# Kernel optimization log

Measured on AMD Instinct MI355X. Metric: run time of the kernel, lower is better.

## Reference

```python
import jax, jax.numpy as jnp
import numpy as np

INPUT_SIZE = 128
HID = 64
B, T = 256, 1024

def setup_inputs() -> dict:
    key = jax.random.key(0)
    ks = jax.random.split(key, 12)
    s1 = 1.0 / np.sqrt(HID)
    def u(k, shape):
        return jax.random.uniform(k, shape, jnp.float32, -s1, s1)
    return {
        "x": jax.random.normal(ks[0], (B, T, INPUT_SIZE), jnp.float32),
        "w_ih0": u(ks[1], (4 * HID, INPUT_SIZE)),
        "w_hh0": u(ks[2], (4 * HID, HID)),
        "b_ih0": u(ks[3], (4 * HID,)),
        "b_hh0": u(ks[4], (4 * HID,)),
        "w_ih1": u(ks[5], (4 * HID, HID)),
        "w_hh1": u(ks[6], (4 * HID, HID)),
        "b_ih1": u(ks[7], (4 * HID,)),
        "b_hh1": u(ks[8], (4 * HID,)),
        "w_out": u(ks[9], (1, HID)),
        "b_out": u(ks[10], (1,)),
    }

def _lstm(x, w_ih, w_hh, b_ih, b_hh):
    # x: [B, T, I] -> h sequence [B, T, H]; PyTorch gate order i, f, g, o
    Bb = x.shape[0]
    H = w_hh.shape[1]
    # precompute input contribution for all timesteps (one big GEMM)
    xg = jnp.einsum('bti,gi->btg', x, w_ih) + b_ih + b_hh  # [B, T, 4H]
    def step(carry, g_t):
        h, c = carry
        g = g_t + h @ w_hh.T  # [B, 4H]
        i, f, gg, o = jnp.split(g, 4, axis=-1)
        i = jax.nn.sigmoid(i)
        f = jax.nn.sigmoid(f)
        gg = jnp.tanh(gg)
        o = jax.nn.sigmoid(o)
        c = f * c + i * gg
        h = o * jnp.tanh(c)
        return (h, c), h
    init = (jnp.zeros((Bb, H), x.dtype), jnp.zeros((Bb, H), x.dtype))
    _, hs = jax.lax.scan(step, init, jnp.swapaxes(xg, 0, 1))  # [T, B, H]
    return jnp.swapaxes(hs, 0, 1)

def reference(x, w_ih0, w_hh0, b_ih0, b_hh0, w_ih1, w_hh1, b_ih1, b_hh1, w_out, b_out):
    h1 = _lstm(x, w_ih0, w_hh0, b_ih0, b_hh0)   # [B, T, H]
    h2 = _lstm(h1, w_ih1, w_hh1, b_ih1, b_hh1)  # [B, T, H]
    logits = jnp.einsum('bth,oh->bto', h2, w_out) + b_out  # [B, T, 1]
    return jax.nn.sigmoid(logits)
```

## Files before the change

kernel.cpp:

```cpp
#include <hip/hip_runtime.h>

#define BB 256
#define TT 1024
#define II 128
#define HH 64
#define BT (BB * TT)

typedef _Float16 h2 __attribute__((ext_vector_type(2)));
typedef _Float16 half8 __attribute__((ext_vector_type(8)));
typedef float f32x4 __attribute__((ext_vector_type(4)));
typedef unsigned int uint;
typedef unsigned short ushort;

#define BC(u) __builtin_bit_cast(h2, (uint)(u))
#define MFMA16(a, b, c) __builtin_amdgcn_mfma_f32_16x16x32_f16((a), (b), (c), 0, 0, 0)
#define SIG(v) __builtin_amdgcn_rcpf(1.0f + __expf(-(v)))
#define TNH(v) (1.0f - 2.0f * __builtin_amdgcn_rcpf(1.0f + __expf(2.0f * (v))))

#define BAR() asm volatile("s_waitcnt lgkmcnt(0)\n\ts_barrier" ::: "memory")

__device__ __forceinline__ uint pk2(float a, float b) {
    h2 h; h[0] = (_Float16)a; h[1] = (_Float16)b;
    return __builtin_bit_cast(uint, h);
}

__global__ __launch_bounds__(256) __attribute__((amdgpu_waves_per_eu(1, 1)))
void lstm2_core(const float* __restrict__ x, const float* __restrict__ w_ih0,
                const float* __restrict__ w_hh0,
                const float* __restrict__ b_ih0, const float* __restrict__ b_hh0,
                const float* __restrict__ w_ih1, const float* __restrict__ w_hh1,
                const float* __restrict__ b_ih1, const float* __restrict__ b_hh1,
                ushort* __restrict__ h1g)
{
    const int bb = blockIdx.x;
    const int w  = threadIdx.x >> 6;
    const int j  = threadIdx.x & 63;
    const int qq = j >> 4, cc = j & 15;
    const int j4 = j * 4;

    __shared__ __align__(16) uint   h0buf[8][32];
    __shared__ __align__(16) uint   h1buf[32];
    __shared__ __align__(16) float  zbuf[8][64][4];
    __shared__ __align__(16) ushort xgb[2][16][264];
    __shared__ __align__(16) uint4  wfrag[16][4][4][16];

    {
        #pragma unroll
        for (int t = 0; t < 16; ++t) {
            const int flat = t * 16 + cc;
            const int srcrow = (flat & 3) * 64 + (flat >> 2);
            const float* p = w_ih0 + (size_t)srcrow * II + w * 32 + qq * 8;
            uint4 v;
            v.x = pk2(p[0], p[1]); v.y = pk2(p[2], p[3]);
            v.z = pk2(p[4], p[5]); v.w = pk2(p[6], p[7]);
            wfrag[t][w][qq][cc] = v;
        }
    }
    __syncthreads();

    uint4 Bf[16][2];
    if (w < 3) {
        const float* Wsel = (w == 0) ? w_hh0 : (w == 1) ? w_ih1 : w_hh1;
        #pragma unroll
        for (int t = 0; t < 16; ++t) {
            const int row = (t & 3) * 64 + (t >> 2) * 16 + cc;
            const float* rp = Wsel + (size_t)row * 64 + qq * 8;
            #pragma unroll
            for (int kh = 0; kh < 2; ++kh) {
                const float* p = rp + kh * 32;
                uint4 v;
                v.x = pk2(p[0], p[1]); v.y = pk2(p[2], p[3]);
                v.z = pk2(p[4], p[5]); v.w = pk2(p[6], p[7]);
                Bf[t][kh] = v;
            }
        }
    }

    float bI = 0.f, bF = 0.f, bG = 0.f, bO = 0.f;
    if (w == 0) {
        bI = b_ih0[j]       + b_hh0[j];
        bF = b_ih0[64 + j]  + b_hh0[64 + j];
        bG = b_ih0[128 + j] + b_hh0[128 + j];
        bO = b_ih0[192 + j] + b_hh0[192 + j];
    } else if (w == 2) {
        bI = b_ih1[j]       + b_hh1[j];
        bF = b_ih1[64 + j]  + b_hh1[64 + j];
        bG = b_ih1[128 + j] + b_hh1[128 + j];
        bO = b_ih1[192 + j] + b_hh1[192 + j];
    }

    float cst = 0.0f;
    const float* xrow = x + (size_t)bb * TT * II;
    ushort* h1b = h1g + (size_t)bb * TT * 64 + j;

    const f32x4 ZR4 = {0.f, 0.f, 0.f, 0.f};
    const int qlo = qq & 1, qhi = qq >> 1;

    half8 af0 = {0,0,0,0,0,0,0,0}, af1 = {0,0,0,0,0,0,0,0};
    f32x4 zr = {0.f, 0.f, 0.f, 0.f};

    float4 xr[8];
    half8 wa0 = {0,0,0,0,0,0,0,0}, wa1 = wa0, wa2 = wa0, wa3 = wa0;

#define XLOAD(WND) if ((WND) < 64) { \
    const float* xp_ = xrow + (size_t)((WND) * 16 + cc) * II + qq * 8; \
    xr[0] = *(const float4*)(xp_ +  0); xr[1] = *(const float4*)(xp_ +  4); \
    xr[2] = *(const float4*)(xp_ + 32); xr[3] = *(const float4*)(xp_ + 36); \
    xr[4] = *(const float4*)(xp_ + 64); xr[5] = *(const float4*)(xp_ + 68); \
    xr[6] = *(const float4*)(xp_ + 96); xr[7] = *(const float4*)(xp_ + 100); }

#define MKAF4() { uint4 u_; \
    u_.x = pk2(xr[0].x, xr[0].y); u_.y = pk2(xr[0].z, xr[0].w); \
    u_.z = pk2(xr[1].x, xr[1].y); u_.w = pk2(xr[1].z, xr[1].w); \
    wa0 = __builtin_bit_cast(half8, u_); \
    u_.x = pk2(xr[2].x, xr[2].y); u_.y = pk2(xr[2].z, xr[2].w); \
    u_.z = pk2(xr[3].x, xr[3].y); u_.w = pk2(xr[3].z, xr[3].w); \
    wa1 = __builtin_bit_cast(half8, u_); \
    u_.x = pk2(xr[4].x, xr[4].y); u_.y = pk2(xr[4].z, xr[4].w); \
    u_.z = pk2(xr[5].x, xr[5].y); u_.w = pk2(xr[5].z, xr[5].w); \
    wa2 = __builtin_bit_cast(half8, u_); \
    u_.x = pk2(xr[6].x, xr[6].y); u_.y = pk2(xr[6].z, xr[6].w); \
    u_.z = pk2(xr[7].x, xr[7].y); u_.w = pk2(xr[7].z, xr[7].w); \
    wa3 = __builtin_bit_cast(half8, u_); }

#define WTILE(TILE, BUF) { \
    f32x4 d_ = ZR4; \
    d_ = MFMA16(wa0, __builtin_bit_cast(half8, wfrag[TILE][0][qq][cc]), d_); \
    d_ = MFMA16(wa1, __builtin_bit_cast(half8, wfrag[TILE][1][qq][cc]), d_); \
    d_ = MFMA16(wa2, __builtin_bit_cast(half8, wfrag[TILE][2][qq][cc]), d_); \
    d_ = MFMA16(wa3, __builtin_bit_cast(half8, wfrag[TILE][3][qq][cc]), d_); \
    _Pragma("unroll") \
    for (int r_ = 0; r_ < 4; ++r_) { \
        _Float16 hv_ = (_Float16)d_[r_]; \
        xgb[BUF][qq * 4 + r_][(TILE) * 16 + cc] = __builtin_bit_cast(ushort, hv_); } }

    if (w == 3) {
        XLOAD(0)
        MKAF4()
        #pragma unroll
        for (int t = 0; t < 16; ++t) WTILE(t, 0)
        XLOAD(1)
    }
    __syncthreads();

#define LDAF(SRC) { const char* hb_ = (const char*)(SRC); \
    af0 = *(const half8*)(hb_ + (qq << 4)); \
    af1 = *(const half8*)(hb_ + 64 + (qq << 4)); }

#define GEMV16(SI, SF, SG, SO) { \
    f32x4 D[16]; \
    _Pragma("unroll") \
    for (int t = 0; t < 16; ++t) { \
        f32x4 d_ = MFMA16(af0, __builtin_bit_cast(half8, Bf[t][0]), ZR4); \
        D[t] = MFMA16(af1, __builtin_bit_cast(half8, Bf[t][1]), d_); } \
    { float a_, b_; \
      a_ = qlo ? D[ 4][0] : D[ 0][0]; b_ = qlo ? D[12][0] : D[ 8][0]; SI = qhi ? b_ : a_; \
      a_ = qlo ? D[ 5][0] : D[ 1][0]; b_ = qlo ? D[13][0] : D[ 9][0]; SF = qhi ? b_ : a_; \
      a_ = qlo ? D[ 6][0] : D[ 2][0]; b_ = qlo ? D[14][0] : D[10][0]; SG = qhi ? b_ : a_; \
      a_ = qlo ? D[ 7][0] : D[ 3][0]; b_ = qlo ? D[15][0] : D[11][0]; SO = qhi ? b_ : a_; } }

#define PSTEP(KK) \
    if ((KK) < TT) { \
        const uint2 xcv = *(const uint2*)&xgb[((KK) >> 4) & 1][(KK) & 15][j4]; \
        float si, sf, sg, so; \
        GEMV16(si, sf, sg, so) \
        h2 xlo = BC(xcv.x), xhi = BC(xcv.y); \
        si += bI + (float)xlo[0]; sf += bF + (float)xlo[1]; \
        sg += bG + (float)xhi[0]; so += bO + (float)xhi[1]; \
        float ii = SIG(si), ff = SIG(sf), gg = TNH(sg), oo = SIG(so); \
        cst = fmaf(ff, cst, ii * gg); \
        float hval = oo * TNH(cst); \
        ((_Float16*)&h0buf[(KK) & 7][0])[j] = (_Float16)hval; \
        LDAF(&h0buf[(KK) & 7][0]) \
    }

#define Q1STEP(KK) { const int i_ = (KK); \
    if (i_ >= 3 && i_ < TT + 3) { \
        const int m_ = i_ - 3; \
        float si, sf, sg, so; \
        GEMV16(si, sf, sg, so) \
        f32x4 zv = {si, sf, sg, so}; \
        *(f32x4*)&zbuf[m_ & 7][j][0] = zv; \
    } \
    if (i_ >= 2 && i_ < TT + 2) LDAF(&h0buf[(i_ - 2) & 7][0]) }

#define Q2STEP(KK) { const int i_ = (KK); \
    if (i_ >= 6) { \
        const int m_ = i_ - 6; \
        float si, sf, sg, so; \
        GEMV16(si, sf, sg, so) \
        si += bI + zr[0]; sf += bF + zr[1]; \
        sg += bG + zr[2]; so += bO + zr[3]; \
        float ii = SIG(si), ff = SIG(sf), gg = TNH(sg), oo = SIG(so); \
        cst = fmaf(ff, cst, ii * gg); \
        float hval = oo * TNH(cst); \
        _Float16 hf = (_Float16)hval; \
        ((_Float16*)&h1buf[0])[j] = hf; \
        LDAF(&h1buf[0]) \
        h1b[(size_t)m_ * 64] = __builtin_bit_cast(ushort, hf); \
    } \
    if (i_ >= 5 && i_ < TT + 5) zr = *(const f32x4*)&zbuf[(i_ - 5) & 7][j][0]; }

    for (int k0 = 0; k0 < TT + 6; k0 += 2) {
        if (w == 0) {
            PSTEP(k0)
            PSTEP(k0 + 1)
        } else if (w == 1) {
            Q1STEP(k0)
            Q1STEP(k0 + 1)
        } else if (w == 2) {
            Q2STEP(k0)
            Q2STEP(k0 + 1)
        } else {
            const int s   = (k0 >> 1) & 7;
            const int wnd = (k0 >> 4) + 1;
            if (s == 0) {
                if (wnd < 64) MKAF4()
                XLOAD(wnd + 1)
            }
            if (wnd < 64) {
                const int buf = wnd & 1;
                WTILE(2 * s,     buf)
                WTILE(2 * s + 1, buf)
            }
        }
        BAR();
    }
#undef PSTEP
#undef Q1STEP
#undef Q2STEP
#undef GEMV16
#undef LDAF
#undef WTILE
#undef MKAF4
#undef XLOAD
}

__global__ __launch_bounds__(256)
void head_gemv(const ushort* __restrict__ h1g, const float* __restrict__ w_out,
               const float* __restrict__ b_out, float* __restrict__ outp)
{
    __shared__ float wsh[64];
    const int tid = threadIdx.x;
    if (tid < 64) wsh[tid] = w_out[tid];
    __syncthreads();
    const int bt = blockIdx.x * 256 + tid;
    const uint4* hp = (const uint4*)(h1g + (size_t)bt * 64);
    float s = 0.0f;
    #pragma unroll
    for (int i = 0; i < 8; ++i) {
        uint4 v = hp[i];
        const float* wp = &wsh[8 * i];
        h2 p;
        p = BC(v.x); s = fmaf((float)p[0], wp[0], s); s = fmaf((float)p[1], wp[1], s);
        p = BC(v.y); s = fmaf((float)p[0], wp[2], s); s = fmaf((float)p[1], wp[3], s);
        p = BC(v.z); s = fmaf((float)p[0], wp[4], s); s = fmaf((float)p[1], wp[5], s);
        p = BC(v.w); s = fmaf((float)p[0], wp[6], s); s = fmaf((float)p[1], wp[7], s);
    }
    outp[bt] = __builtin_amdgcn_rcpf(1.0f + __expf(-(s + b_out[0])));
}

extern "C" void kernel_launch(void* const* d_in, const int* in_sizes, int n_in,
                              void* d_out, int out_size, void* d_ws, size_t ws_size,
                              hipStream_t stream) {
    const float* x     = (const float*)d_in[0];
    const float* w_ih0 = (const float*)d_in[1];
    const float* w_hh0 = (const float*)d_in[2];
    const float* b_ih0 = (const float*)d_in[3];
    const float* b_hh0 = (const float*)d_in[4];
    const float* w_ih1 = (const float*)d_in[5];
    const float* w_hh1 = (const float*)d_in[6];
    const float* b_ih1 = (const float*)d_in[7];
    const float* b_hh1 = (const float*)d_in[8];
    const float* w_out = (const float*)d_in[9];
    const float* b_out = (const float*)d_in[10];
    float* out = (float*)d_out;

    ushort* h1g = (ushort*)d_ws;

    hipLaunchKernelGGL(lstm2_core, dim3(BB), dim3(256), 0, stream,
                       x, w_ih0, w_hh0, b_ih0, b_hh0,
                       w_ih1, w_hh1, b_ih1, b_hh1, h1g);
    hipLaunchKernelGGL(head_gemv, dim3(BT / 256), dim3(256), 0, stream,
                       h1g, w_out, b_out, out);
}
```

Baseline: 800.6 us.

## Split each LSTM role across two waves, halving per-step MFMA chain

Doubles the block to 512 threads so that each role (layer-0 recurrence, layer-1 input projection, layer-1 recurrence, x-projection producer) is shared by two waves, each computing half of the 64 hidden units with 8 instead of 16 MFMA tiles. The software pipeline is reworked to one timestep per barrier with double-buffered h0/h1/z buffers and a shallower skew (k-1, k-2), so each wave sees a shorter critical path per step. The cost is a barrier every step instead of every two steps, twice as many waves competing for each SIMD, and half of each wave's lanes doing redundant gate math that is then discarded.

```diff
diff --git a/kernel.cpp b/kernel.cpp
--- a/kernel.cpp
+++ b/kernel.cpp
@@ -24,7 +24,7 @@
     return __builtin_bit_cast(uint, h);
 }
 
-__global__ __launch_bounds__(256) __attribute__((amdgpu_waves_per_eu(1, 1)))
+__global__ __launch_bounds__(512) __attribute__((amdgpu_waves_per_eu(2, 2)))
 void lstm2_core(const float* __restrict__ x, const float* __restrict__ w_ih0,
                 const float* __restrict__ w_hh0,
                 const float* __restrict__ b_ih0, const float* __restrict__ b_hh0,
@@ -32,38 +32,46 @@
                 const float* __restrict__ b_ih1, const float* __restrict__ b_hh1,
                 ushort* __restrict__ h1g)
 {
-    const int bb = blockIdx.x;
-    const int w  = threadIdx.x >> 6;
-    const int j  = threadIdx.x & 63;
-    const int qq = j >> 4, cc = j & 15;
-    const int j4 = j * 4;
-
-    __shared__ __align__(16) uint   h0buf[8][32];
-    __shared__ __align__(16) uint   h1buf[32];
-    __shared__ __align__(16) float  zbuf[8][64][4];
+    const int bb   = blockIdx.x;
+    const int tid  = threadIdx.x;
+    const int w    = tid >> 6;
+    const int role = w >> 1;
+    const int wh   = w & 1;
+    const int ln   = tid & 63;
+    const int qq   = ln >> 4, cc = ln & 15;
+    const int jl   = ln & 31;
+    const int j    = wh * 32 + jl;
+    const int sel  = (ln >> 4) & 1;
+    const bool lo32 = (ln < 32);
+
+    __shared__ __align__(16) uint   h0buf[2][32];
+    __shared__ __align__(16) uint   h1buf[2][32];
+    __shared__ __align__(16) float  zbuf[2][64][4];
     __shared__ __align__(16) ushort xgb[2][16][264];
     __shared__ __align__(16) uint4  wfrag[16][4][4][16];
 
     {
+        const int kc = w & 3;
         #pragma unroll
-        for (int t = 0; t < 16; ++t) {
-            const int flat = t * 16 + cc;
+        for (int t = 0; t < 8; ++t) {
+            const int T = (w >> 2) * 8 + t;
+            const int flat = T * 16 + cc;
             const int srcrow = (flat & 3) * 64 + (flat >> 2);
-            const float* p = w_ih0 + (size_t)srcrow * II + w * 32 + qq * 8;
+            const float* p = w_ih0 + (size_t)srcrow * II + kc * 32 + qq * 8;
             uint4 v;
             v.x = pk2(p[0], p[1]); v.y = pk2(p[2], p[3]);
             v.z = pk2(p[4], p[5]); v.w = pk2(p[6], p[7]);
-            wfrag[t][w][qq][cc] = v;
+            wfrag[T][kc][qq][cc] = v;
         }
     }
-    __syncthreads();
-
-    uint4 Bf[16][2];
-    if (w < 3) {
-        const float* Wsel = (w == 0) ? w_hh0 : (w == 1) ? w_ih1 : w_hh1;
+
+    uint4 Bf[8][2];
+    if (role < 3) {
+        const float* Wsel = (role == 0) ? w_hh0 : (role == 1) ? w_ih1 : w_hh1;
         #pragma unroll
-        for (int t = 0; t < 16; ++t) {
-            const int row = (t & 3) * 64 + (t >> 2) * 16 + cc;
+        for (int t = 0; t < 8; ++t) {
+            const int T = wh * 8 + t;
+            const int row = (T & 3) * 64 + (T >> 2) * 16 + cc;
             const float* rp = Wsel + (size_t)row * 64 + qq * 8;
             #pragma unroll
             for (int kh = 0; kh < 2; ++kh) {
@@ -77,12 +85,12 @@
     }
 
     float bI = 0.f, bF = 0.f, bG = 0.f, bO = 0.f;
-    if (w == 0) {
+    if (role == 0) {
         bI = b_ih0[j]       + b_hh0[j];
         bF = b_ih0[64 + j]  + b_hh0[64 + j];
         bG = b_ih0[128 + j] + b_hh0[128 + j];
         bO = b_ih0[192 + j] + b_hh0[192 + j];
-    } else if (w == 2) {
+    } else if (role == 2) {
         bI = b_ih1[j]       + b_hh1[j];
         bF = b_ih1[64 + j]  + b_hh1[64 + j];
         bG = b_ih1[128 + j] + b_hh1[128 + j];
@@ -94,13 +102,10 @@
     ushort* h1b = h1g + (size_t)bb * TT * 64 + j;
 
     const f32x4 ZR4 = {0.f, 0.f, 0.f, 0.f};
-    const int qlo = qq & 1, qhi = qq >> 1;
-
-    half8 af0 = {0,0,0,0,0,0,0,0}, af1 = {0,0,0,0,0,0,0,0};
-    f32x4 zr = {0.f, 0.f, 0.f, 0.f};
-
-    float4 xr[8];
-    half8 wa0 = {0,0,0,0,0,0,0,0}, wa1 = wa0, wa2 = wa0, wa3 = wa0;
+
+    half8 af0 = {0,0,0,0,0,0,0,0}, af1 = af0;
+    float4 xr[8] = {};
+    half8 wa0 = af0, wa1 = af0, wa2 = af0, wa3 = af0;
 
 #define XLOAD(WND) if ((WND) < 64) { \
     const float* xp_ = xrow + (size_t)((WND) * 16 + cc) * II + qq * 8; \
@@ -123,115 +128,104 @@
     u_.z = pk2(xr[7].x, xr[7].y); u_.w = pk2(xr[7].z, xr[7].w); \
     wa3 = __builtin_bit_cast(half8, u_); }
 
-#define WTILE(TILE, BUF) { \
+#define WTILEH(T, BUF) { \
     f32x4 d_ = ZR4; \
-    d_ = MFMA16(wa0, __builtin_bit_cast(half8, wfrag[TILE][0][qq][cc]), d_); \
-    d_ = MFMA16(wa1, __builtin_bit_cast(half8, wfrag[TILE][1][qq][cc]), d_); \
-    d_ = MFMA16(wa2, __builtin_bit_cast(half8, wfrag[TILE][2][qq][cc]), d_); \
-    d_ = MFMA16(wa3, __builtin_bit_cast(half8, wfrag[TILE][3][qq][cc]), d_); \
+    d_ = MFMA16(wa0, __builtin_bit_cast(half8, wfrag[T][0][qq][cc]), d_); \
+    d_ = MFMA16(wa1, __builtin_bit_cast(half8, wfrag[T][1][qq][cc]), d_); \
+    d_ = MFMA16(wa2, __builtin_bit_cast(half8, wfrag[T][2][qq][cc]), d_); \
+    d_ = MFMA16(wa3, __builtin_bit_cast(half8, wfrag[T][3][qq][cc]), d_); \
     _Pragma("unroll") \
     for (int r_ = 0; r_ < 4; ++r_) { \
         _Float16 hv_ = (_Float16)d_[r_]; \
-        xgb[BUF][qq * 4 + r_][(TILE) * 16 + cc] = __builtin_bit_cast(ushort, hv_); } }
-
-    if (w == 3) {
+        xgb[BUF][qq * 4 + r_][(T) * 16 + cc] = __builtin_bit_cast(ushort, hv_); } }
+
+    __syncthreads();
+    if (role == 3) {
         XLOAD(0)
         MKAF4()
         #pragma unroll
-        for (int t = 0; t < 16; ++t) WTILE(t, 0)
+        for (int t = 0; t < 8; ++t) WTILEH(wh * 8 + t, 0)
         XLOAD(1)
-    }
+    } else if (tid < 32)       h0buf[1][tid] = 0u;
+    else if (tid >= 64 && tid < 96) h1buf[1][tid - 64] = 0u;
     __syncthreads();
 
 #define LDAF(SRC) { const char* hb_ = (const char*)(SRC); \
     af0 = *(const half8*)(hb_ + (qq << 4)); \
     af1 = *(const half8*)(hb_ + 64 + (qq << 4)); }
 
-#define GEMV16(SI, SF, SG, SO) { \
-    f32x4 D[16]; \
+#define GEMV8(SI, SF, SG, SO) { \
+    f32x4 D[8]; \
     _Pragma("unroll") \
-    for (int t = 0; t < 16; ++t) { \
+    for (int t = 0; t < 8; ++t) { \
         f32x4 d_ = MFMA16(af0, __builtin_bit_cast(half8, Bf[t][0]), ZR4); \
         D[t] = MFMA16(af1, __builtin_bit_cast(half8, Bf[t][1]), d_); } \
-    { float a_, b_; \
-      a_ = qlo ? D[ 4][0] : D[ 0][0]; b_ = qlo ? D[12][0] : D[ 8][0]; SI = qhi ? b_ : a_; \
-      a_ = qlo ? D[ 5][0] : D[ 1][0]; b_ = qlo ? D[13][0] : D[ 9][0]; SF = qhi ? b_ : a_; \
-      a_ = qlo ? D[ 6][0] : D[ 2][0]; b_ = qlo ? D[14][0] : D[10][0]; SG = qhi ? b_ : a_; \
-      a_ = qlo ? D[ 7][0] : D[ 3][0]; b_ = qlo ? D[15][0] : D[11][0]; SO = qhi ? b_ : a_; } }
-
-#define PSTEP(KK) \
-    if ((KK) < TT) { \
-        const uint2 xcv = *(const uint2*)&xgb[((KK) >> 4) & 1][(KK) & 15][j4]; \
-        float si, sf, sg, so; \
-        GEMV16(si, sf, sg, so) \
-        h2 xlo = BC(xcv.x), xhi = BC(xcv.y); \
-        si += bI + (float)xlo[0]; sf += bF + (float)xlo[1]; \
-        sg += bG + (float)xhi[0]; so += bO + (float)xhi[1]; \
-        float ii = SIG(si), ff = SIG(sf), gg = TNH(sg), oo = SIG(so); \
-        cst = fmaf(ff, cst, ii * gg); \
-        float hval = oo * TNH(cst); \
-        ((_Float16*)&h0buf[(KK) & 7][0])[j] = (_Float16)hval; \
-        LDAF(&h0buf[(KK) & 7][0]) \
-    }
-
-#define Q1STEP(KK) { const int i_ = (KK); \
-    if (i_ >= 3 && i_ < TT + 3) { \
-        const int m_ = i_ - 3; \
-        float si, sf, sg, so; \
-        GEMV16(si, sf, sg, so) \
-        f32x4 zv = {si, sf, sg, so}; \
-        *(f32x4*)&zbuf[m_ & 7][j][0] = zv; \
-    } \
-    if (i_ >= 2 && i_ < TT + 2) LDAF(&h0buf[(i_ - 2) & 7][0]) }
-
-#define Q2STEP(KK) { const int i_ = (KK); \
-    if (i_ >= 6) { \
-        const int m_ = i_ - 6; \
-        float si, sf, sg, so; \
-        GEMV16(si, sf, sg, so) \
-        si += bI + zr[0]; sf += bF + zr[1]; \
-        sg += bG + zr[2]; so += bO + zr[3]; \
-        float ii = SIG(si), ff = SIG(sf), gg = TNH(sg), oo = SIG(so); \
-        cst = fmaf(ff, cst, ii * gg); \
-        float hval = oo * TNH(cst); \
-        _Float16 hf = (_Float16)hval; \
-        ((_Float16*)&h1buf[0])[j] = hf; \
-        LDAF(&h1buf[0]) \
-        h1b[(size_t)m_ * 64] = __builtin_bit_cast(ushort, hf); \
-    } \
-    if (i_ >= 5 && i_ < TT + 5) zr = *(const f32x4*)&zbuf[(i_ - 5) & 7][j][0]; }
-
-    for (int k0 = 0; k0 < TT + 6; k0 += 2) {
-        if (w == 0) {
-            PSTEP(k0)
-            PSTEP(k0 + 1)
-        } else if (w == 1) {
-            Q1STEP(k0)
-            Q1STEP(k0 + 1)
-        } else if (w == 2) {
-            Q2STEP(k0)
-            Q2STEP(k0 + 1)
+    SI = sel ? D[4][0] : D[0][0]; \
+    SF = sel ? D[5][0] : D[1][0]; \
+    SG = sel ? D[6][0] : D[2][0]; \
+    SO = sel ? D[7][0] : D[3][0]; }
+
+    for (int k = 0; k < TT + 2; ++k) {
+        if (role == 0) {
+            if (k < TT) {
+                LDAF(&h0buf[(k + 1) & 1][0])
+                const uint2 xcv = *(const uint2*)&xgb[(k >> 4) & 1][k & 15][j * 4];
+                float si, sf, sg, so;
+                GEMV8(si, sf, sg, so)
+                h2 xlo = BC(xcv.x), xhi = BC(xcv.y);
+                si += bI + (float)xlo[0]; sf += bF + (float)xlo[1];
+                sg += bG + (float)xhi[0]; so += bO + (float)xhi[1];
+                float ii = SIG(si), ff = SIG(sf), gg = TNH(sg), oo = SIG(so);
+                cst = fmaf(ff, cst, ii * gg);
+                float hval = oo * TNH(cst);
+                if (lo32) ((_Float16*)&h0buf[k & 1][0])[j] = (_Float16)hval;
+            }
+        } else if (role == 1) {
+            if (k >= 1 && k <= TT) {
+                const int m = k - 1;
+                LDAF(&h0buf[m & 1][0])
+                float si, sf, sg, so;
+                GEMV8(si, sf, sg, so)
+                if (lo32) {
+                    f32x4 zv = {si, sf, sg, so};
+                    *(f32x4*)&zbuf[m & 1][j][0] = zv;
+                }
+            }
+        } else if (role == 2) {
+            if (k >= 2) {
+                const int m = k - 2;
+                LDAF(&h1buf[(m + 1) & 1][0])
+                const f32x4 zr = *(const f32x4*)&zbuf[m & 1][j][0];
+                float si, sf, sg, so;
+                GEMV8(si, sf, sg, so)
+                si += bI + zr[0]; sf += bF + zr[1];
+                sg += bG + zr[2]; so += bO + zr[3];
+                float ii = SIG(si), ff = SIG(sf), gg = TNH(sg), oo = SIG(so);
+                cst = fmaf(ff, cst, ii * gg);
+                float hval = oo * TNH(cst);
+                _Float16 hf = (_Float16)hval;
+                if (lo32) {
+                    ((_Float16*)&h1buf[m & 1][0])[j] = hf;
+                    h1b[(size_t)m * 64] = __builtin_bit_cast(ushort, hf);
+                }
+            }
         } else {
-            const int s   = (k0 >> 1) & 7;
-            const int wnd = (k0 >> 4) + 1;
-            if (s == 0) {
-                if (wnd < 64) MKAF4()
+            const int sl = k & 15;
+            const int wnd = (k >> 4) + 1;
+            if (sl == 0) {
+                if (wnd < 64) { MKAF4() }
                 XLOAD(wnd + 1)
             }
-            if (wnd < 64) {
-                const int buf = wnd & 1;
-                WTILE(2 * s,     buf)
-                WTILE(2 * s + 1, buf)
+            if (wnd < 64 && !(sl & 1)) {
+                const int t = sl >> 1;
+                WTILEH(wh * 8 + t, wnd & 1)
             }
         }
         BAR();
     }
-#undef PSTEP
-#undef Q1STEP
-#undef Q2STEP
-#undef GEMV16
+#undef GEMV8
 #undef LDAF
-#undef WTILE
+#undef WTILEH
 #undef MKAF4
 #undef XLOAD
 }
@@ -278,7 +272,7 @@
 
     ushort* h1g = (ushort*)d_ws;
 
-    hipLaunchKernelGGL(lstm2_core, dim3(BB), dim3(256), 0, stream,
+    hipLaunchKernelGGL(lstm2_core, dim3(BB), dim3(512), 0, stream,
                        x, w_ih0, w_hh0, b_ih0, b_hh0,
                        w_ih1, w_hh1, b_ih1, b_hh1, h1g);
     hipLaunchKernelGGL(head_gemv, dim3(BT / 256), dim3(256), 0, stream,
```

Measured after the change: 1.003 ms. 25.3% more time.
